# Kernel tuning notes

Hardware: AMD Instinct MI355X
Metric: run time of the kernel (lower is better)

Reference implementation:

```python
import jax, jax.numpy as jnp
import numpy as np

B, L, D = 4, 2048, 64
N_HEAD = 4
LOCALITY = 0.2
PI = 3.141592653589793


def setup_inputs() -> dict:
    key = jax.random.key(0)
    k1, k2, k3 = jax.random.split(key, 3)
    mesh = jax.random.uniform(k1, (B, L, 2), dtype=jnp.float32)
    inputs = jax.random.normal(k2, (B, L, D), dtype=jnp.float32)
    lmda = jax.random.uniform(k3, (N_HEAD, 1, 1), dtype=jnp.float32)
    return {"mesh": mesh, "inputs": inputs, "lmda": lmda}


def reference(mesh, inputs, lmda):
    FMAX = jnp.finfo(jnp.float32).max
    # pairwise squared distances: (B, L, L)
    diff = mesh[:, :, None, :] - mesh[:, None, :, :]
    m_dist = jnp.sum(diff * diff, axis=-1)
    # per-head scale in (0, inf): tan(pi/4 * (1-eps) * (1 + sin(lmda)))
    scale = jnp.tan(0.25 * PI * (1.0 - 1e-07) * (1.0 + jnp.sin(lmda)))  # (H,1,1)
    scaled = m_dist[:, None, :, :] * scale  # (B, H, L, L)
    # row-wise quantile threshold (linear interpolation, matching torch.quantile)
    thresh = jnp.quantile(scaled, LOCALITY, axis=-1, keepdims=True)  # (B,H,L,1)
    masked = jnp.where(scaled <= thresh, scaled, FMAX)
    att = jax.nn.softmax(-masked, axis=-1)  # (B, H, L, L)
    # aggregate: (B,H,L,L) x (B,L,D) -> (B,L,H,D) -> (B,L,H*D)
    conv = jnp.einsum('bhnj,bjd->bnhd', att, inputs)
    conv = conv.reshape(inputs.shape[0], -1, N_HEAD * inputs.shape[-1])
    return jnp.concatenate([inputs, conv], axis=-1)
```

## Files before the change

kernel.cpp:

```cpp
#include <hip/hip_runtime.h>
#include <math.h>

#ifndef M_PI
#define M_PI 3.14159265358979323846
#endif

namespace {
constexpr int B_ = 4;
constexpr int L_ = 2048;
constexpr int D_ = 64;
constexpr int H_ = 4;
constexpr int RB = 8;
constexpr int KT = 64;
constexpr int NTILE = L_ / KT;
constexpr int CAPC = 256;
constexpr int OUTW = D_ + H_ * D_;
constexpr int APS = 2064;
constexpr int ABYTES = 2 * APS;
constexpr int BBYTES = KT * D_ * 2;
constexpr int BUFB = ABYTES + BBYTES;
}

typedef __attribute__((ext_vector_type(8))) short bf16x8;
typedef __attribute__((ext_vector_type(4))) float f32x4;

__device__ __forceinline__ unsigned bf16_rne(float x) {
    unsigned u = __float_as_uint(x);
    return (u + 0x7fffu + ((u >> 16) & 1u)) >> 16;
}

__device__ __forceinline__ unsigned cvt_pk_bf16(float lo, float hi) {
    unsigned r;
    asm("v_cvt_pk_bf16_f32 %0, %1, %2" : "=v"(r) : "v"(lo), "v"(hi));
    return r;
}

#if defined(__has_builtin)
#if __has_builtin(__builtin_amdgcn_exp2f)
#define EXP2F(x) __builtin_amdgcn_exp2f(x)
#endif
#endif
#ifndef EXP2F
#define EXP2F(x) __expf((x) * 0.69314718055994531f)
#endif

#define LDS_FENCE() __builtin_amdgcn_s_waitcnt(0xC07F)

__global__ __launch_bounds__(256) void prep_thresh_kernel(
    const float* __restrict__ mesh,
    const float* __restrict__ inputs,
    char* __restrict__ ws,
    float* __restrict__ out)
{
    __shared__ unsigned s_hist[4][256];
    __shared__ float s_cand[4][256];

    const int t = threadIdx.x;
    const int l = t & 63;
    const int w = t >> 6;
    const int blk = blockIdx.x;

    if (t < 128) {
        const unsigned u = (unsigned)blk * 128u + (unsigned)t;
        const int pb = u >> 16;
        const int rem = u & 65535;
        const int tile = rem >> 12;
        const int idx = rem & 4095;
        const int n = idx & 63;
        const int kl = (idx >> 6) << 1;
        const float* inb = inputs + ((size_t)pb * L_ + tile * 128) * D_;
        char* wsb = ws + (size_t)pb * (L_ * D_ * 2) + tile * (128 * D_ * 2);
        const float x0 = inb[kl * D_ + n];
        const float x1 = inb[(kl + 1) * D_ + n];
        const int chunk = (kl >> 3) * 64 + n;
        const int e = kl & 7;
        *reinterpret_cast<unsigned*>(wsb + chunk * 16 + e * 2) =
            bf16_rne(x0) | (bf16_rne(x1) << 16);
    }

    const int row = blk * 4 + w;
    const int b = row >> 11;
    const int rl = row & 2047;
    const float2* meshg = reinterpret_cast<const float2*>(mesh) + (size_t)b * L_;
    unsigned* hw = s_hist[w];
    float* cw = s_cand[w];
    const float2 me = meshg[rl];

    *reinterpret_cast<uint4*>(&hw[l * 4]) = make_uint4(0u, 0u, 0u, 0u);
    LDS_FENCE();
    #pragma unroll 4
    for (int it = 0; it < 32; ++it) {
        const int j = (it << 6) + l;
        const float2 mj = meshg[j];
        const float dx = __fsub_rn(me.x, mj.x);
        const float dy = __fsub_rn(me.y, mj.y);
        const float d = __fadd_rn(__fmul_rn(dx, dx), __fmul_rn(dy, dy));
        int bin = (int)(d * 128.0f); bin = bin < 255 ? bin : 255;
        atomicAdd(&hw[bin], 1u);
    }
    LDS_FENCE();
    int lo, hi; unsigned base;
    {
        const uint4 hv = *reinterpret_cast<const uint4*>(&hw[l * 4]);
        const unsigned p0 = hv.x, p1 = p0 + hv.y, p2 = p1 + hv.z, p3 = p2 + hv.w;
        unsigned sc = p3;
        #pragma unroll
        for (int off = 1; off < 64; off <<= 1) {
            const unsigned uu = __shfl_up(sc, off);
            if (l >= off) sc += uu;
        }
        const unsigned eb = sc - p3;
        const unsigned cum[4] = {eb + p0, eb + p1, eb + p2, eb + p3};
        int flo = -1, fhi = -1; unsigned fbase = 0u;
        #pragma unroll
        for (int e = 0; e < 4; ++e) {
            const unsigned prev = e ? cum[e - 1] : eb;
            if (cum[e] > 409u && prev <= 409u) { flo = l * 4 + e; fbase = prev; }
            if (cum[e] > 410u && prev <= 410u) { fhi = l * 4 + e; }
        }
        const unsigned long long bmlo = __ballot(flo >= 0);
        const int srclo = (int)__builtin_ctzll(bmlo);
        lo = __shfl(flo, srclo);
        base = __shfl(fbase, srclo);
        const unsigned long long bmhi = __ballot(fhi >= 0);
        hi = __shfl(fhi, (int)__builtin_ctzll(bmhi));
    }
    unsigned cbase = 0u;
    #pragma unroll 4
    for (int it = 0; it < 32; ++it) {
        const int j = (it << 6) + l;
        const float2 mj = meshg[j];
        const float dx = __fsub_rn(me.x, mj.x);
        const float dy = __fsub_rn(me.y, mj.y);
        const float d = __fadd_rn(__fmul_rn(dx, dx), __fmul_rn(dy, dy));
        int bin = (int)(d * 128.0f); bin = bin < 255 ? bin : 255;
        const bool pred = (bin >= lo && bin <= hi);
        const unsigned long long bm = __ballot(pred);
        if (pred) {
            const unsigned p = cbase + (unsigned)__popcll(bm & ((1ull << l) - 1ull));
            if (p < (unsigned)CAPC) cw[p] = d;
        }
        cbase += (unsigned)__popcll(bm);
    }
    LDS_FENCE();
    const int m = (int)min(cbase, (unsigned)CAPC);
    const unsigned k409 = 409u - base;
    const unsigned k410 = 410u - base;
    const float lo_edge = (float)lo * 0.0078125f;
    const float sc2 = 32768.0f / (float)(hi - lo + 1);
    *reinterpret_cast<uint4*>(&hw[l * 4]) = make_uint4(0u, 0u, 0u, 0u);
    LDS_FENCE();
    #pragma unroll 2
    for (int ci = l; ci < m; ci += 64) {
        const float v = cw[ci];
        int b2 = (int)(__fmul_rn(__fsub_rn(v, lo_edge), sc2));
        b2 = b2 < 255 ? b2 : 255; b2 = b2 > 0 ? b2 : 0;
        atomicAdd(&hw[b2], 1u);
    }
    LDS_FENCE();
    int lo2, hi2; unsigned base2;
    {
        const uint4 hv = *reinterpret_cast<const uint4*>(&hw[l * 4]);
        const unsigned p0 = hv.x, p1 = p0 + hv.y, p2 = p1 + hv.z, p3 = p2 + hv.w;
        unsigned sc = p3;
        #pragma unroll
        for (int off = 1; off < 64; off <<= 1) {
            const unsigned uu = __shfl_up(sc, off);
            if (l >= off) sc += uu;
        }
        const unsigned eb = sc - p3;
        const unsigned cum[4] = {eb + p0, eb + p1, eb + p2, eb + p3};
        int flo = -1, fhi = -1; unsigned fbase = 0u;
        #pragma unroll
        for (int e = 0; e < 4; ++e) {
            const unsigned prev = e ? cum[e - 1] : eb;
            if (cum[e] > k409 && prev <= k409) { flo = l * 4 + e; fbase = prev; }
            if (cum[e] > k410 && prev <= k410) { fhi = l * 4 + e; }
        }
        const unsigned long long bmlo = __ballot(flo >= 0);
        const int srclo = (int)__builtin_ctzll(bmlo);
        lo2 = __shfl(flo, srclo);
        base2 = __shfl(fbase, srclo);
        const unsigned long long bmhi = __ballot(fhi >= 0);
        hi2 = __shfl(fhi, (int)__builtin_ctzll(bmhi));
    }
    float* c2 = reinterpret_cast<float*>(hw);
    unsigned cnt2 = 0u;
    for (int c0 = 0; c0 < m; c0 += 64) {
        const int ci = c0 + l;
        float v = 0.0f; bool pred = false;
        if (ci < m) {
            v = cw[ci];
            int b2 = (int)(__fmul_rn(__fsub_rn(v, lo_edge), sc2));
            b2 = b2 < 255 ? b2 : 255; b2 = b2 > 0 ? b2 : 0;
            pred = (b2 >= lo2 && b2 <= hi2);
        }
        const unsigned long long bm = __ballot(pred);
        if (pred) {
            const unsigned p = cnt2 + (unsigned)__popcll(bm & ((1ull << l) - 1ull));
            if (p < 256u) c2[p] = v;
        }
        cnt2 += (unsigned)__popcll(bm);
    }
    LDS_FENCE();
    const int c = (int)min(cnt2, 256u);
    const int q409 = (int)(k409 - base2);
    const int q410 = (int)(k410 - base2);
    if (l == 0) { cw[0] = 0.0f; cw[1] = 0.0f; }
    LDS_FENCE();
    #pragma unroll 1
    for (int cc0 = 0; cc0 < c; cc0 += 64) {
        const int ci = cc0 + l;
        const float v = (ci < c) ? c2[ci] : 0.0f;
        int lt = 0, le = 0;
        #pragma unroll 4
        for (int i = 0; i < c; ++i) {
            const float u = c2[i];
            lt += (u < v) ? 1 : 0;
            le += (u <= v) ? 1 : 0;
        }
        if (ci < c) {
            if (lt <= q409 && q409 < le) cw[0] = v;
            if (lt <= q410 && q410 < le) cw[1] = v;
        }
    }
    LDS_FENCE();
    if (l == 0) {
        const float d409 = cw[0], d410 = cw[1];
        const float pos = 0.2f * 2047.0f;
        const float g = pos - 409.0f;
        const float lw = 1.0f - g;
        const float thD = __fadd_rn(__fmul_rn(d409, lw), __fmul_rn(d410, g));
        out[(size_t)(b * L_ + rl) * OUTW + 319] = thD;
    }
}

__global__ __launch_bounds__(512, 8) void posatt_kernel(
    const float* __restrict__ mesh,
    const float* __restrict__ inputs,
    const float* __restrict__ lmda,
    const char* __restrict__ ws,
    float* __restrict__ out)
{
    __shared__ __align__(16) char s_u1[2 * BUFB];
    __shared__ float s_scale[H_];
    __shared__ float s_thD[RB];
    __shared__ float s_wsum[RB][H_];

    const int t = threadIdx.x;
    const int l = t & 63;
    const int w = t >> 6;
    const int blk = blockIdx.x;
    const int b = blk >> 8;
    const int n0 = (blk & 255) * RB;

    const float2* meshg = reinterpret_cast<const float2*>(mesh) + (size_t)b * L_;

    if (t < H_) {
        const double lam = (double)lmda[t];
        const float C = (float)(0.25 * M_PI * (1.0 - 1e-07));
        const float s1 = (float)sin(lam);
        const float arg = __fmul_rn(C, __fadd_rn(1.0f, s1));
        s_scale[t] = (float)tan((double)arg);
    }
    if (t < RB) {
        s_thD[t] = out[(size_t)(b * L_ + n0 + t) * OUTW + 319];
    }
    __syncthreads();

    const int jp = t & 31;
    const int rr = (t >> 5) & 7;
    const int h2 = t >> 8;
    const float2 me_b = meshg[n0 + rr];
    const float thD = s_thD[rr];
    constexpr float LOG2E = 1.4426950408889634f;
    const float cA = __fmul_rn(-LOG2E, s_scale[h2]);
    const float cB = __fmul_rn(-LOG2E, s_scale[h2 + 2]);
    const int row16 = h2 * 8 + rr;
    const int ks4q_w = jp >> 2;
    const int chunk_w = ks4q_w * 16 + row16;
    const int chunkSw_w = chunk_w ^ (ks4q_w & 7);
    const int aoff0 = (chunkSw_w << 4) + ((jp & 3) << 2);
    float waccA = 0.0f, waccB = 0.0f;

    const int p_w  = w >> 2;
    const int ks_w = (w >> 1) & 1;
    const int nqh  = w & 1;
    const int ks4q_r = ks_w * 4 + (l >> 4);
    const int chunk_r = ks4q_r * 16 + (l & 15);
    const int aroff = p_w * APS + ((chunk_r ^ (ks4q_r & 7)) << 4);
    f32x4 acc[2];
    acc[0] = (f32x4)0.0f; acc[1] = (f32x4)0.0f;

    const float* inpb = inputs + (size_t)b * L_ * D_;
    const char* wsb = ws + (size_t)b * (L_ * D_ * 2);
    const float4* mesh4 = reinterpret_cast<const float4*>(meshg);
    char* const AE = s_u1;
    char* const BE = s_u1 + ABYTES;
    char* const AO = s_u1 + BUFB;
    char* const BO = s_u1 + BUFB + ABYTES;

    auto LOADB = [&](int tile) -> uint4 {
        return *reinterpret_cast<const uint4*>(wsb + ((size_t)(tile * 512 + t) << 4));
    };
    auto COMMITB = [&](char* Bb, const uint4 bg) {
        *reinterpret_cast<uint4*>(Bb + (t << 4)) = bg;
    };
    auto ABUILD = [&](int tile, char* Ab) {
        const float4 mq = mesh4[tile * 32 + jp];
        const float dx0 = __fsub_rn(me_b.x, mq.x);
        const float dy0 = __fsub_rn(me_b.y, mq.y);
        const float d0 = __fadd_rn(__fmul_rn(dx0, dx0), __fmul_rn(dy0, dy0));
        const float dx1 = __fsub_rn(me_b.x, mq.z);
        const float dy1 = __fsub_rn(me_b.y, mq.w);
        const float d1 = __fadd_rn(__fmul_rn(dx1, dx1), __fmul_rn(dy1, dy1));
        const bool pass0 = (d0 <= thD);
        const bool pass1 = (d1 <= thD);
        const float wA0 = pass0 ? EXP2F(__fmul_rn(d0, cA)) : 0.0f;
        const float wA1 = pass1 ? EXP2F(__fmul_rn(d1, cA)) : 0.0f;
        const float wB0 = pass0 ? EXP2F(__fmul_rn(d0, cB)) : 0.0f;
        const float wB1 = pass1 ? EXP2F(__fmul_rn(d1, cB)) : 0.0f;
        waccA += __fadd_rn(wA0, wA1);
        waccB += __fadd_rn(wB0, wB1);
        *reinterpret_cast<unsigned*>(Ab + aoff0) = cvt_pk_bf16(wA0, wA1);
        *reinterpret_cast<unsigned*>(Ab + APS + aoff0) = cvt_pk_bf16(wB0, wB1);
    };
    auto MFMA_STEP = [&](const char* Ab, const char* Bb) {
        const bf16x8 afr = *reinterpret_cast<const bf16x8*>(Ab + aroff);
        #pragma unroll
        for (int i = 0; i < 2; ++i) {
            const int nq = nqh * 2 + i;
            const bf16x8 bfr = *reinterpret_cast<const bf16x8*>(
                Bb + (((ks_w * 4 + (l >> 4)) * 64 + nq * 16 + (l & 15)) << 4));
            acc[i] = __builtin_amdgcn_mfma_f32_16x16x32_bf16(afr, bfr, acc[i], 0, 0, 0);
        }
    };

    {
        const uint4 bg0 = LOADB(0);
        ABUILD(0, AE);
        COMMITB(BE, bg0);
    }
    __syncthreads();
    #pragma unroll 1
    for (int tp = 0; tp < NTILE / 2; ++tp) {
        uint4 bg = LOADB(2 * tp + 1);
        MFMA_STEP(AE, BE);
        ABUILD(2 * tp + 1, AO);
        COMMITB(BO, bg);
        __syncthreads();
        if (tp < NTILE / 2 - 1) {
            bg = LOADB(2 * tp + 2);
            MFMA_STEP(AO, BO);
            ABUILD(2 * tp + 2, AE);
            COMMITB(BE, bg);
            __syncthreads();
        }
    }
    MFMA_STEP(AO, BO);
    __syncthreads();

    waccA += __shfl_xor(waccA, 1);
    waccA += __shfl_xor(waccA, 2);
    waccA += __shfl_xor(waccA, 4);
    waccA += __shfl_xor(waccA, 8);
    waccA += __shfl_xor(waccA, 16);
    waccB += __shfl_xor(waccB, 1);
    waccB += __shfl_xor(waccB, 2);
    waccB += __shfl_xor(waccB, 4);
    waccB += __shfl_xor(waccB, 8);
    waccB += __shfl_xor(waccB, 16);
    if ((l & 31) == 0) {
        s_wsum[rr][h2] = waccA;
        s_wsum[rr][h2 + 2] = waccB;
    }
    {
        float4* Cz = reinterpret_cast<float4*>(s_u1);
        Cz[t] = make_float4(0.f, 0.f, 0.f, 0.f);
    }
    __syncthreads();
    {
        float* Cf = reinterpret_cast<float*>(s_u1);
        #pragma unroll
        for (int i = 0; i < 2; ++i) {
            const int nq = nqh * 2 + i;
            #pragma unroll
            for (int reg = 0; reg < 4; ++reg) {
                const int row = (l >> 4) * 4 + reg;
                const int col = nq * 16 + (l & 15);
                atomicAdd(&Cf[(p_w * 16 + row) * 64 + col], acc[i][reg]);
            }
        }
    }
    __syncthreads();
    {
        const float* Cf = reinterpret_cast<const float*>(s_u1);
        const int pr = t >> 4;
        const int p = pr >> 4;
        const int row16o = pr & 15;
        const int h = p * 2 + (row16o >> 3);
        const int r = row16o & 7;
        const int col = (t & 15) << 2;
        const float wsv = s_wsum[r][h];
        const float inv = (wsv != 0.0f) ? 1.0f / wsv : 0.0f;
        float4 r0 = *reinterpret_cast<const float4*>(&Cf[pr * 64 + col]);
        r0.x *= inv; r0.y *= inv; r0.z *= inv; r0.w *= inv;
        float* op = out + (size_t)(b * L_ + n0 + r) * OUTW + D_ + h * 64 + col;
        *reinterpret_cast<float4*>(op) = r0;
    }
    {
        const int r = t >> 6;
        const int c = t & 63;
        out[(size_t)(b * L_ + n0 + r) * OUTW + c] = inpb[(size_t)(n0 + r) * D_ + c];
    }
}

extern "C" void kernel_launch(void* const* d_in, const int* in_sizes, int n_in,
                              void* d_out, int out_size, void* d_ws, size_t ws_size,
                              hipStream_t stream) {
    const float* mesh   = (const float*)d_in[0];
    const float* inputs = (const float*)d_in[1];
    const float* lmda   = (const float*)d_in[2];
    float* out = (float*)d_out;
    char* ws = (char*)d_ws;
    (void)in_sizes; (void)n_in; (void)out_size; (void)ws_size;
    hipLaunchKernelGGL(prep_thresh_kernel, dim3(2048), dim3(256), 0, stream,
                       mesh, inputs, ws, out);
    hipLaunchKernelGGL(posatt_kernel, dim3(B_ * (L_ / RB)), dim3(512), 0, stream,
                       mesh, inputs, lmda, ws, out);
}
```

Measured before the change: 128.6 us.

## Build MFMA operands in registers directly, removing LDS staging and barriers

The main attention kernel now has each wave compute its softmax weights straight into the MFMA A-operand registers and load B fragments from global memory into registers, with one-tile register prefetch. This removes the double-buffered LDS tiles and the per-tile __syncthreads. The block shrinks to 256 threads with four accumulators per wave. Block indices are remapped so each XCD handles one batch half, which should improve L2 locality. The trade-off is more redundant exp work per wave, since each wave recomputes weights for its own k-slice, plus higher register pressure and uncoalesced 16-byte global loads.

```diff
diff --git a/kernel.cpp b/kernel.cpp
--- a/kernel.cpp
+++ b/kernel.cpp
@@ -15,10 +15,6 @@
 constexpr int NTILE = L_ / KT;
 constexpr int CAPC = 256;
 constexpr int OUTW = D_ + H_ * D_;
-constexpr int APS = 2064;
-constexpr int ABYTES = 2 * APS;
-constexpr int BBYTES = KT * D_ * 2;
-constexpr int BUFB = ABYTES + BBYTES;
 }
 
 typedef __attribute__((ext_vector_type(8))) short bf16x8;
@@ -235,24 +231,28 @@
     }
 }
 
-__global__ __launch_bounds__(512, 8) void posatt_kernel(
+__global__ __launch_bounds__(256, 4) void posatt_kernel(
     const float* __restrict__ mesh,
     const float* __restrict__ inputs,
     const float* __restrict__ lmda,
     const char* __restrict__ ws,
     float* __restrict__ out)
 {
-    __shared__ __align__(16) char s_u1[2 * BUFB];
+    __shared__ float s_C[32 * 64];
     __shared__ float s_scale[H_];
     __shared__ float s_thD[RB];
-    __shared__ float s_wsum[RB][H_];
+    __shared__ float s_ws2[2][2][16];
 
     const int t = threadIdx.x;
     const int l = t & 63;
     const int w = t >> 6;
+    const int p_w  = w >> 1;
+    const int ks_w = w & 1;
+
     const int blk = blockIdx.x;
-    const int b = blk >> 8;
-    const int n0 = (blk & 255) * RB;
+    const int xcd = blk & 7;
+    const int b = xcd >> 1;
+    const int n0 = (((xcd & 1) << 7) + (blk >> 3)) * RB;
 
     const float2* meshg = reinterpret_cast<const float2*>(mesh) + (size_t)b * L_;
 
@@ -268,150 +268,112 @@
     }
     __syncthreads();
 
-    const int jp = t & 31;
-    const int rr = (t >> 5) & 7;
-    const int h2 = t >> 8;
-    const float2 me_b = meshg[n0 + rr];
-    const float thD = s_thD[rr];
+    const int row16 = l & 15;
+    const int kq = l >> 4;
+    const int rl = row16 & 7;
+    const float2 me = meshg[n0 + rl];
+    const float thD = s_thD[rl];
     constexpr float LOG2E = 1.4426950408889634f;
-    const float cA = __fmul_rn(-LOG2E, s_scale[h2]);
-    const float cB = __fmul_rn(-LOG2E, s_scale[h2 + 2]);
-    const int row16 = h2 * 8 + rr;
-    const int ks4q_w = jp >> 2;
-    const int chunk_w = ks4q_w * 16 + row16;
-    const int chunkSw_w = chunk_w ^ (ks4q_w & 7);
-    const int aoff0 = (chunkSw_w << 4) + ((jp & 3) << 2);
-    float waccA = 0.0f, waccB = 0.0f;
-
-    const int p_w  = w >> 2;
-    const int ks_w = (w >> 1) & 1;
-    const int nqh  = w & 1;
-    const int ks4q_r = ks_w * 4 + (l >> 4);
-    const int chunk_r = ks4q_r * 16 + (l & 15);
-    const int aroff = p_w * APS + ((chunk_r ^ (ks4q_r & 7)) << 4);
-    f32x4 acc[2];
+    const float cH = __fmul_rn(-LOG2E, s_scale[p_w * 2 + (row16 >> 3)]);
+
+    const char* bptr = ws + (size_t)b * (L_ * D_ * 2)
+                     + ((size_t)(((ks_w * 4 + kq) * 64) + row16) << 4);
+    const float4* mptr = reinterpret_cast<const float4*>(meshg) + (ks_w * 16 + kq * 4);
+
+    f32x4 acc[4];
     acc[0] = (f32x4)0.0f; acc[1] = (f32x4)0.0f;
-
+    acc[2] = (f32x4)0.0f; acc[3] = (f32x4)0.0f;
+    float wacc = 0.0f;
+
+    uint4 cb0, cb1, cb2, cb3;
+    float4 cm0, cm1, cm2, cm3;
+    auto LOADT = [&](int tl, uint4& B0, uint4& B1, uint4& B2, uint4& B3,
+                     float4& M0, float4& M1, float4& M2, float4& M3) {
+        const char* p = bptr + ((size_t)tl << 13);
+        B0 = *reinterpret_cast<const uint4*>(p);
+        B1 = *reinterpret_cast<const uint4*>(p + 256);
+        B2 = *reinterpret_cast<const uint4*>(p + 512);
+        B3 = *reinterpret_cast<const uint4*>(p + 768);
+        const float4* q = mptr + tl * 32;
+        M0 = q[0]; M1 = q[1]; M2 = q[2]; M3 = q[3];
+    };
+    auto DW = [&](float mx, float my) -> float {
+        const float dx = __fsub_rn(me.x, mx);
+        const float dy = __fsub_rn(me.y, my);
+        const float d = __fadd_rn(__fmul_rn(dx, dx), __fmul_rn(dy, dy));
+        const float x = __fmul_rn(d, cH);
+        return (d <= thD) ? EXP2F(x) : 0.0f;
+    };
+    auto STEP = [&]() {
+        const float w0 = DW(cm0.x, cm0.y), w1 = DW(cm0.z, cm0.w);
+        const float w2 = DW(cm1.x, cm1.y), w3 = DW(cm1.z, cm1.w);
+        const float w4 = DW(cm2.x, cm2.y), w5 = DW(cm2.z, cm2.w);
+        const float w6 = DW(cm3.x, cm3.y), w7 = DW(cm3.z, cm3.w);
+        wacc = __fadd_rn(wacc,
+            __fadd_rn(__fadd_rn(__fadd_rn(w0, w1), __fadd_rn(w2, w3)),
+                      __fadd_rn(__fadd_rn(w4, w5), __fadd_rn(w6, w7))));
+        union { uint4 u; bf16x8 v; } av;
+        av.u = make_uint4(cvt_pk_bf16(w0, w1), cvt_pk_bf16(w2, w3),
+                          cvt_pk_bf16(w4, w5), cvt_pk_bf16(w6, w7));
+        union { uint4 u; bf16x8 v; } b0v, b1v, b2v, b3v;
+        b0v.u = cb0; b1v.u = cb1; b2v.u = cb2; b3v.u = cb3;
+        acc[0] = __builtin_amdgcn_mfma_f32_16x16x32_bf16(av.v, b0v.v, acc[0], 0, 0, 0);
+        acc[1] = __builtin_amdgcn_mfma_f32_16x16x32_bf16(av.v, b1v.v, acc[1], 0, 0, 0);
+        acc[2] = __builtin_amdgcn_mfma_f32_16x16x32_bf16(av.v, b2v.v, acc[2], 0, 0, 0);
+        acc[3] = __builtin_amdgcn_mfma_f32_16x16x32_bf16(av.v, b3v.v, acc[3], 0, 0, 0);
+    };
+
+    LOADT(0, cb0, cb1, cb2, cb3, cm0, cm1, cm2, cm3);
+    #pragma unroll 1
+    for (int tl = 0; tl < NTILE - 1; ++tl) {
+        uint4 nb0, nb1, nb2, nb3;
+        float4 nm0, nm1, nm2, nm3;
+        LOADT(tl + 1, nb0, nb1, nb2, nb3, nm0, nm1, nm2, nm3);
+        STEP();
+        cb0 = nb0; cb1 = nb1; cb2 = nb2; cb3 = nb3;
+        cm0 = nm0; cm1 = nm1; cm2 = nm2; cm3 = nm3;
+    }
+    STEP();
+
+    wacc += __shfl_xor(wacc, 16);
+    wacc += __shfl_xor(wacc, 32);
+    if (l < 16) s_ws2[ks_w][p_w][l] = wacc;
+    {
+        float4* Cz = reinterpret_cast<float4*>(s_C);
+        Cz[t] = make_float4(0.f, 0.f, 0.f, 0.f);
+        Cz[t + 256] = make_float4(0.f, 0.f, 0.f, 0.f);
+    }
+    __syncthreads();
+    #pragma unroll
+    for (int nq = 0; nq < 4; ++nq) {
+        #pragma unroll
+        for (int reg = 0; reg < 4; ++reg) {
+            const int row = kq * 4 + reg;
+            const int col = nq * 16 + row16;
+            atomicAdd(&s_C[(p_w * 16 + row) * 64 + col], acc[nq][reg]);
+        }
+    }
+    __syncthreads();
     const float* inpb = inputs + (size_t)b * L_ * D_;
-    const char* wsb = ws + (size_t)b * (L_ * D_ * 2);
-    const float4* mesh4 = reinterpret_cast<const float4*>(meshg);
-    char* const AE = s_u1;
-    char* const BE = s_u1 + ABYTES;
-    char* const AO = s_u1 + BUFB;
-    char* const BO = s_u1 + BUFB + ABYTES;
-
-    auto LOADB = [&](int tile) -> uint4 {
-        return *reinterpret_cast<const uint4*>(wsb + ((size_t)(tile * 512 + t) << 4));
-    };
-    auto COMMITB = [&](char* Bb, const uint4 bg) {
-        *reinterpret_cast<uint4*>(Bb + (t << 4)) = bg;
-    };
-    auto ABUILD = [&](int tile, char* Ab) {
-        const float4 mq = mesh4[tile * 32 + jp];
-        const float dx0 = __fsub_rn(me_b.x, mq.x);
-        const float dy0 = __fsub_rn(me_b.y, mq.y);
-        const float d0 = __fadd_rn(__fmul_rn(dx0, dx0), __fmul_rn(dy0, dy0));
-        const float dx1 = __fsub_rn(me_b.x, mq.z);
-        const float dy1 = __fsub_rn(me_b.y, mq.w);
-        const float d1 = __fadd_rn(__fmul_rn(dx1, dx1), __fmul_rn(dy1, dy1));
-        const bool pass0 = (d0 <= thD);
-        const bool pass1 = (d1 <= thD);
-        const float wA0 = pass0 ? EXP2F(__fmul_rn(d0, cA)) : 0.0f;
-        const float wA1 = pass1 ? EXP2F(__fmul_rn(d1, cA)) : 0.0f;
-        const float wB0 = pass0 ? EXP2F(__fmul_rn(d0, cB)) : 0.0f;
-        const float wB1 = pass1 ? EXP2F(__fmul_rn(d1, cB)) : 0.0f;
-        waccA += __fadd_rn(wA0, wA1);
-        waccB += __fadd_rn(wB0, wB1);
-        *reinterpret_cast<unsigned*>(Ab + aoff0) = cvt_pk_bf16(wA0, wA1);
-        *reinterpret_cast<unsigned*>(Ab + APS + aoff0) = cvt_pk_bf16(wB0, wB1);
-    };
-    auto MFMA_STEP = [&](const char* Ab, const char* Bb) {
-        const bf16x8 afr = *reinterpret_cast<const bf16x8*>(Ab + aroff);
-        #pragma unroll
-        for (int i = 0; i < 2; ++i) {
-            const int nq = nqh * 2 + i;
-            const bf16x8 bfr = *reinterpret_cast<const bf16x8*>(
-                Bb + (((ks_w * 4 + (l >> 4)) * 64 + nq * 16 + (l & 15)) << 4));
-            acc[i] = __builtin_amdgcn_mfma_f32_16x16x32_bf16(afr, bfr, acc[i], 0, 0, 0);
-        }
-    };
-
-    {
-        const uint4 bg0 = LOADB(0);
-        ABUILD(0, AE);
-        COMMITB(BE, bg0);
-    }
-    __syncthreads();
-    #pragma unroll 1
-    for (int tp = 0; tp < NTILE / 2; ++tp) {
-        uint4 bg = LOADB(2 * tp + 1);
-        MFMA_STEP(AE, BE);
-        ABUILD(2 * tp + 1, AO);
-        COMMITB(BO, bg);
-        __syncthreads();
-        if (tp < NTILE / 2 - 1) {
-            bg = LOADB(2 * tp + 2);
-            MFMA_STEP(AO, BO);
-            ABUILD(2 * tp + 2, AE);
-            COMMITB(BE, bg);
-            __syncthreads();
-        }
-    }
-    MFMA_STEP(AO, BO);
-    __syncthreads();
-
-    waccA += __shfl_xor(waccA, 1);
-    waccA += __shfl_xor(waccA, 2);
-    waccA += __shfl_xor(waccA, 4);
-    waccA += __shfl_xor(waccA, 8);
-    waccA += __shfl_xor(waccA, 16);
-    waccB += __shfl_xor(waccB, 1);
-    waccB += __shfl_xor(waccB, 2);
-    waccB += __shfl_xor(waccB, 4);
-    waccB += __shfl_xor(waccB, 8);
-    waccB += __shfl_xor(waccB, 16);
-    if ((l & 31) == 0) {
-        s_wsum[rr][h2] = waccA;
-        s_wsum[rr][h2 + 2] = waccB;
-    }
-    {
-        float4* Cz = reinterpret_cast<float4*>(s_u1);
-        Cz[t] = make_float4(0.f, 0.f, 0.f, 0.f);
-    }
-    __syncthreads();
-    {
-        float* Cf = reinterpret_cast<float*>(s_u1);
-        #pragma unroll
-        for (int i = 0; i < 2; ++i) {
-            const int nq = nqh * 2 + i;
-            #pragma unroll
-            for (int reg = 0; reg < 4; ++reg) {
-                const int row = (l >> 4) * 4 + reg;
-                const int col = nq * 16 + (l & 15);
-                atomicAdd(&Cf[(p_w * 16 + row) * 64 + col], acc[i][reg]);
-            }
-        }
-    }
-    __syncthreads();
-    {
-        const float* Cf = reinterpret_cast<const float*>(s_u1);
-        const int pr = t >> 4;
+    #pragma unroll
+    for (int half = 0; half < 2; ++half) {
+        const int s = t + half * 256;
+        const int pr = s >> 4;
         const int p = pr >> 4;
-        const int row16o = pr & 15;
-        const int h = p * 2 + (row16o >> 3);
-        const int r = row16o & 7;
-        const int col = (t & 15) << 2;
-        const float wsv = s_wsum[r][h];
+        const int r16 = pr & 15;
+        const int h = p * 2 + (r16 >> 3);
+        const int r = r16 & 7;
+        const int col = (s & 15) << 2;
+        const float wsv = s_ws2[0][p][r16] + s_ws2[1][p][r16];
         const float inv = (wsv != 0.0f) ? 1.0f / wsv : 0.0f;
-        float4 r0 = *reinterpret_cast<const float4*>(&Cf[pr * 64 + col]);
+        float4 r0 = *reinterpret_cast<const float4*>(&s_C[pr * 64 + col]);
         r0.x *= inv; r0.y *= inv; r0.z *= inv; r0.w *= inv;
         float* op = out + (size_t)(b * L_ + n0 + r) * OUTW + D_ + h * 64 + col;
         *reinterpret_cast<float4*>(op) = r0;
-    }
-    {
-        const int r = t >> 6;
-        const int c = t & 63;
-        out[(size_t)(b * L_ + n0 + r) * OUTW + c] = inpb[(size_t)(n0 + r) * D_ + c];
+        const int rr2 = s >> 6;
+        const int cc2 = s & 63;
+        out[(size_t)(b * L_ + n0 + rr2) * OUTW + cc2] =
+            inpb[(size_t)(n0 + rr2) * D_ + cc2];
     }
 }
 
@@ -426,6 +388,6 @@
     (void)in_sizes; (void)n_in; (void)out_size; (void)ws_size;
     hipLaunchKernelGGL(prep_thresh_kernel, dim3(2048), dim3(256), 0, stream,
                        mesh, inputs, ws, out);
-    hipLaunchKernelGGL(posatt_kernel, dim3(B_ * (L_ / RB)), dim3(512), 0, stream,
+    hipLaunchKernelGGL(posatt_kernel, dim3(B_ * (L_ / RB)), dim3(256), 0, stream,
                        mesh, inputs, lmda, ws, out);
 }
```

After: 127.0 us. No clear change (-1.2%).
